# Performance work log

Measured on AMD Instinct MI355X. Metric: run time of the kernel, lower is better.

## Reference

```python
import jax, jax.numpy as jnp
import numpy as np

N_NODES = 100000
N_EDGES = 1200000
D = 64          # hidden_feat_dim == out_feat_dim
D_CELL = 16     # cell_feat_dim
HID = 256       # MLP hidden width (from MLP(..., 256, ...))
N_TGT = 50000


def setup_inputs() -> dict:
    key = jax.random.key(0)
    ks = jax.random.split(key, 13)
    inv = lambda d: 1.0 / np.sqrt(d)
    return {
        "h": jax.random.normal(ks[0], (N_NODES, D), jnp.float32),
        "cell_feat": jax.random.normal(ks[1], (N_NODES, D_CELL), jnp.float32),
        "src": jax.random.randint(ks[2], (N_EDGES,), 0, N_NODES, jnp.int32),
        "dst": jax.random.randint(ks[3], (N_EDGES,), 0, N_NODES, jnp.int32),
        "targets": jax.random.randint(ks[4], (N_TGT,), 0, N_NODES, jnp.int32),
        "Wn1": jax.random.normal(ks[5], (D, HID), jnp.float32) * inv(D),
        "bn1": jnp.zeros((HID,), jnp.float32),
        "Wn2": jax.random.normal(ks[6], (HID, D), jnp.float32) * inv(HID),
        "bn2": jnp.zeros((D,), jnp.float32),
        "Ws1": jax.random.normal(ks[7], (D_CELL, HID), jnp.float32) * inv(D_CELL),
        "bs1": jnp.zeros((HID,), jnp.float32),
        "Ws2": jax.random.normal(ks[8], (HID, D), jnp.float32) * inv(HID),
        "bs2": jnp.zeros((D,), jnp.float32),
    }


def _mlp2(x, W1, b1, W2, b2):
    # MLP(d_in, 256, d_out) with LeakyReLU(negative_slope=0) == ReLU
    return jax.nn.relu(x @ W1 + b1) @ W2 + b2


def reference(h, cell_feat, src, dst, targets,
              Wn1, bn1, Wn2, bn2, Ws1, bs1, Ws2, bs2):
    # PathConv forward, even level_id > 0, flag_attn=False:
    #   pull(copy_src('h','m'), cell_msg_reduce, apply_cell_func) on 'cell' edges
    N = h.shape[0]
    m = h[src]  # gather edge messages [E, D]
    # cell_msg_reduce: per-dst, per-channel softmax over incoming messages
    mmax = jax.ops.segment_max(m, dst, num_segments=N)          # [N, D]
    mmax = jnp.where(jnp.isfinite(mmax), mmax, 0.0)             # isolated nodes
    e = jnp.exp(m - mmax[dst])                                  # [E, D]
    den = jax.ops.segment_sum(e, dst, num_segments=N)           # [N, D]
    num = jax.ops.segment_sum(e * m, dst, num_segments=N)       # sum(msg*softmax)
    h_neigh1 = num / jnp.where(den == 0.0, 1.0, den)            # [N, D]
    # apply_cell_func: fc_cell_self(cell_feat) + fc_cell_neigh(h_neigh1)
    h_new = _mlp2(cell_feat, Ws1, bs1, Ws2, bs2) + _mlp2(h_neigh1, Wn1, bn1, Wn2, bn2)
    h_new = jax.nn.relu(h_new)  # self.activation
    return h_new[targets]
```

## Files before the change

kernel.cpp:

```cpp
#include <hip/hip_runtime.h>

#define NN 100000
#define NE 1200000
#define DD 64
#define DC 16
#define DH 256
#define NT 50000
#define MAXDEG 64

typedef __attribute__((ext_vector_type(8))) short bf16x8;
typedef __attribute__((ext_vector_type(4))) short bf16x4;
typedef __attribute__((ext_vector_type(4))) float f32x4;

__device__ __forceinline__ unsigned short f2bf(float x) {
    unsigned int u = __float_as_uint(x);
    return (unsigned short)((u + 0x7FFFu + ((u >> 16) & 1u)) >> 16);
}
__device__ __forceinline__ float bf2f(unsigned short b) {
    return __uint_as_float(((unsigned int)b) << 16);
}

__device__ __forceinline__ void split8r(const float* p, bf16x8& hi, bf16x8& lo) {
    f32x4 a = *reinterpret_cast<const f32x4*>(p);
    f32x4 b = *reinterpret_cast<const f32x4*>(p + 4);
    #pragma unroll
    for (int j = 0; j < 4; ++j) {
        unsigned short h = f2bf(a[j]);
        hi[j] = (short)h;
        lo[j] = (short)f2bf(a[j] - bf2f(h));
    }
    #pragma unroll
    for (int j = 0; j < 4; ++j) {
        unsigned short h = f2bf(b[j]);
        hi[4 + j] = (short)h;
        lo[4 + j] = (short)f2bf(b[j] - bf2f(h));
    }
}

__device__ __forceinline__ bf16x8 zero8() {
    return bf16x8{0, 0, 0, 0, 0, 0, 0, 0};
}
__device__ __forceinline__ bf16x8 pad8(bf16x4 v) {
    return bf16x8{v[0], v[1], v[2], v[3], 0, 0, 0, 0};
}

__global__ __launch_bounds__(256) void mark_wl_k(
    const int* __restrict__ tg, int* __restrict__ ifl, int* __restrict__ cnt)
{
    int i = blockIdx.x * 256 + threadIdx.x;
    int lane = threadIdx.x & 63;
    bool claim = false;
    int t = 0;
    if (i < NT) {
        t = tg[i];
        claim = (atomicCAS(&ifl[t], -1, -2) == -1);
    }
    unsigned long long mask = __ballot(claim);
    if (mask == 0ull) return;
    int nclaim = __popcll(mask);
    int leader = __ffsll((unsigned long long)mask) - 1;
    int base = 0;
    if (lane == leader) base = atomicAdd(cnt, nclaim);
    base = __shfl(base, leader);
    if (claim) {
        int rank = __popcll(mask & ((1ull << lane) - 1ull));
        ifl[t] = base + rank;
    }
}

__global__ __launch_bounds__(256) void scatter_k(
    const int* __restrict__ src, const int* __restrict__ dst,
    const int* __restrict__ ifl, int* __restrict__ deg, int* __restrict__ csr)
{
    int e = blockIdx.x * 256 + threadIdx.x;
    if (e >= NE) return;
    int d = dst[e];
    int w = ifl[d];
    if (w >= 0) {
        int slot = atomicAdd(&deg[w], 1);
        if (slot < MAXDEG) csr[w * MAXDEG + slot] = src[e];
    }
}

__global__ __launch_bounds__(256) void reduce_k(
    const float* __restrict__ h, const int* __restrict__ csr,
    const int* __restrict__ deg, const int* __restrict__ cnt,
    float* __restrict__ hn_c)
{
    int gw = (blockIdx.x * 256 + threadIdx.x) >> 6;
    int lane = threadIdx.x & 63;
    if (gw >= cnt[0]) return;
    int g = min(deg[gw], MAXDEG);
    int sid = csr[gw * MAXDEG + lane];
    if (lane >= g) sid = 0;
    const int e4 = lane >> 4, c4 = lane & 15;

    f32x4 accd = {0.f, 0.f, 0.f, 0.f}, accn = {0.f, 0.f, 0.f, 0.f};
    for (int base = 0; base < g; base += 16) {
        f32x4 m[4];
        bool  val[4];
        #pragma unroll
        for (int bb = 0; bb < 4; ++bb) {
            int idx = base + bb * 4 + e4;
            val[bb] = (idx < g);
            if (base + bb * 4 < g) {
                int s = __shfl(sid, idx);
                m[bb] = *reinterpret_cast<const f32x4*>(
                            h + (size_t)s * DD + c4 * 4);
            } else {
                m[bb] = f32x4{0.f, 0.f, 0.f, 0.f};
                val[bb] = false;
            }
        }
        #pragma unroll
        for (int bb = 0; bb < 4; ++bb) {
            #pragma unroll
            for (int r = 0; r < 4; ++r) {
                float ex = __expf(m[bb][r]);
                ex = val[bb] ? ex : 0.f;
                accd[r] += ex;
                accn[r] = fmaf(ex, m[bb][r], accn[r]);
            }
        }
    }
    #pragma unroll
    for (int r = 0; r < 4; ++r) {
        accd[r] += __shfl_xor(accd[r], 16);
        accn[r] += __shfl_xor(accn[r], 16);
        accd[r] += __shfl_xor(accd[r], 32);
        accn[r] += __shfl_xor(accn[r], 32);
    }
    if (lane < 16) {
        f32x4 o;
        #pragma unroll
        for (int r = 0; r < 4; ++r)
            o[r] = (accd[r] == 0.f) ? 0.f : accn[r] / accd[r];
        *reinterpret_cast<f32x4*>(hn_c + (size_t)gw * DD + c4 * 4) = o;
    }
}

#define N_W1NT 16384
#define N_W1ST 8192
#define N_W2N  16384
#define N_W2S  16384
#define N_PACK (N_W1NT + N_W1ST + N_W2N + N_W2S)

__global__ __launch_bounds__(256) void pack_w_k(
    const float* __restrict__ Wn1, const float* __restrict__ Ws1,
    const float* __restrict__ Wn2, const float* __restrict__ Ws2,
    unsigned short* __restrict__ W1nT_hi, unsigned short* __restrict__ W1nT_lo,
    unsigned short* __restrict__ W1sT_hi, unsigned short* __restrict__ W1sT_lo,
    unsigned short* __restrict__ W2n_hi,  unsigned short* __restrict__ W2n_lo,
    unsigned short* __restrict__ W2s_hi,  unsigned short* __restrict__ W2s_lo)
{
    int tid = blockIdx.x * 256 + threadIdx.x;
    if (tid >= N_PACK) return;
    float v; unsigned short *ph, *pl; int idx;
    if (tid < N_W1NT) {
        idx = tid;
        int j = idx & 7, l = (idx >> 3) & 63, rest = idx >> 9;
        int ks = rest & 1, c = rest >> 1;
        int feat = ks * 32 + ((l >> 4) << 3) + j, hid = (c << 4) + (l & 15);
        v = Wn1[(size_t)feat * DH + hid];
        ph = W1nT_hi; pl = W1nT_lo;
    } else if (tid < N_W1NT + N_W1ST) {
        idx = tid - N_W1NT;
        int j = idx & 7, l = (idx >> 3) & 63, c = idx >> 9;
        int k = ((l >> 4) << 3) + j, hid = (c << 4) + (l & 15);
        v = (k < DC) ? Ws1[(size_t)k * DH + hid] : 0.0f;
        ph = W1sT_hi; pl = W1sT_lo;
    } else if (tid < N_W1NT + N_W1ST + N_W2N) {
        idx = tid - N_W1NT - N_W1ST;
        int j = idx & 3, l = (idx >> 2) & 63, rest = idx >> 8;
        int u = rest & 3, c = rest >> 2;
        int row = (c << 4) + ((l >> 4) << 2) + j, col = (u << 4) + (l & 15);
        v = Wn2[(size_t)row * DD + col];
        ph = W2n_hi; pl = W2n_lo;
    } else {
        idx = tid - N_W1NT - N_W1ST - N_W2N;
        int j = idx & 3, l = (idx >> 2) & 63, rest = idx >> 8;
        int u = rest & 3, c = rest >> 2;
        int row = (c << 4) + ((l >> 4) << 2) + j, col = (u << 4) + (l & 15);
        v = Ws2[(size_t)row * DD + col];
        ph = W2s_hi; pl = W2s_lo;
    }
    unsigned short hh = f2bf(v);
    ph[idx] = hh;
    pl[idx] = f2bf(v - bf2f(hh));
}

__global__ __launch_bounds__(256, 4) void mfma_mlp_k(
    const float* __restrict__ hn_c, const int* __restrict__ ifl,
    const float* __restrict__ cellf, const int* __restrict__ tg,
    const unsigned short* __restrict__ W1nT_hi, const unsigned short* __restrict__ W1nT_lo,
    const unsigned short* __restrict__ W1sT_hi, const unsigned short* __restrict__ W1sT_lo,
    const unsigned short* __restrict__ W2n_hi,  const unsigned short* __restrict__ W2n_lo,
    const unsigned short* __restrict__ W2s_hi,  const unsigned short* __restrict__ W2s_lo,
    const float* __restrict__ bn1, const float* __restrict__ bs1,
    const float* __restrict__ bn2, const float* __restrict__ bs2,
    float* __restrict__ out)
{
    __shared__ float X[32][84];
    __shared__ float Ys[4][16][68];

    const int tid = threadIdx.x;
    const int wv = tid >> 6, ln = tid & 63;
    const int l16 = ln & 15, kb = (ln >> 4) << 3;
    const int rbase = blockIdx.x * 32;

    {
        int r = tid >> 3, seg = tid & 7;
        int row = rbase + r; if (row >= NT) row = NT - 1;
        int t = tg[row];
        int w = ifl[t];
        const float* hp = hn_c + (size_t)w * DD + seg * 8;
        *reinterpret_cast<f32x4*>(&X[r][seg * 8])     = *reinterpret_cast<const f32x4*>(hp);
        *reinterpret_cast<f32x4*>(&X[r][seg * 8 + 4]) = *reinterpret_cast<const f32x4*>(hp + 4);
        if (tid < 128) {
            int r2 = tid >> 2, q = tid & 3;
            int row2 = rbase + r2; if (row2 >= NT) row2 = NT - 1;
            int t2 = tg[row2];
            *reinterpret_cast<f32x4*>(&X[r2][64 + q * 4]) =
                *reinterpret_cast<const f32x4*>(cellf + (size_t)t2 * DC + q * 4);
        }
    }
    __syncthreads();

    f32x4 accY[2][4];
    #pragma unroll
    for (int g = 0; g < 2; ++g)
        #pragma unroll
        for (int u = 0; u < 4; ++u) accY[g][u] = f32x4{0.f, 0.f, 0.f, 0.f};

    {
        bf16x8 xh[2][2], xl[2][2];
        #pragma unroll
        for (int g = 0; g < 2; ++g)
            #pragma unroll
            for (int ks = 0; ks < 2; ++ks)
                split8r(&X[g * 16 + l16][ks * 32 + kb], xh[g][ks], xl[g][ks]);

        #pragma unroll
        for (int cc = 0; cc < 4; ++cc) {
            int cg = (wv << 2) + cc;
            f32x4 b1 = *reinterpret_cast<const f32x4*>(bn1 + cg * 16 + ((ln >> 4) << 2));
            f32x4 a1[2] = {b1, b1};
            #pragma unroll
            for (int ks = 0; ks < 2; ++ks) {
                bf16x8 wh = *reinterpret_cast<const bf16x8*>(W1nT_hi + (((cg * 2 + ks) * 64 + ln) << 3));
                bf16x8 wl = *reinterpret_cast<const bf16x8*>(W1nT_lo + (((cg * 2 + ks) * 64 + ln) << 3));
                #pragma unroll
                for (int g = 0; g < 2; ++g) {
                    a1[g] = __builtin_amdgcn_mfma_f32_16x16x32_bf16(wh, xh[g][ks], a1[g], 0, 0, 0);
                    a1[g] = __builtin_amdgcn_mfma_f32_16x16x32_bf16(wl, xh[g][ks], a1[g], 0, 0, 0);
                    a1[g] = __builtin_amdgcn_mfma_f32_16x16x32_bf16(wh, xl[g][ks], a1[g], 0, 0, 0);
                }
            }
            bf16x8 pah[2], pal[2];
            #pragma unroll
            for (int g = 0; g < 2; ++g) {
                pah[g] = zero8(); pal[g] = zero8();
                #pragma unroll
                for (int r = 0; r < 4; ++r) {
                    float d = fmaxf(a1[g][r], 0.f);
                    unsigned short hh = f2bf(d);
                    pah[g][r] = (short)hh;
                    pal[g][r] = (short)f2bf(d - bf2f(hh));
                }
            }
            #pragma unroll
            for (int u = 0; u < 4; ++u) {
                bf16x8 w2h = pad8(*reinterpret_cast<const bf16x4*>(W2n_hi + (((cg * 4 + u) * 64 + ln) << 2)));
                bf16x8 w2l = pad8(*reinterpret_cast<const bf16x4*>(W2n_lo + (((cg * 4 + u) * 64 + ln) << 2)));
                #pragma unroll
                for (int g = 0; g < 2; ++g) {
                    accY[g][u] = __builtin_amdgcn_mfma_f32_16x16x32_bf16(pah[g], w2h, accY[g][u], 0, 0, 0);
                    accY[g][u] = __builtin_amdgcn_mfma_f32_16x16x32_bf16(pal[g], w2h, accY[g][u], 0, 0, 0);
                    accY[g][u] = __builtin_amdgcn_mfma_f32_16x16x32_bf16(pah[g], w2l, accY[g][u], 0, 0, 0);
                }
            }
        }
    }

    {
        bf16x8 sxh[2], sxl[2];
        #pragma unroll
        for (int g = 0; g < 2; ++g) { sxh[g] = zero8(); sxl[g] = zero8(); }
        if (ln < 32) {
            #pragma unroll
            for (int g = 0; g < 2; ++g)
                split8r(&X[g * 16 + l16][64 + kb], sxh[g], sxl[g]);
        }
        #pragma unroll
        for (int cc = 0; cc < 4; ++cc) {
            int cg = (wv << 2) + cc;
            f32x4 b1 = *reinterpret_cast<const f32x4*>(bs1 + cg * 16 + ((ln >> 4) << 2));
            f32x4 a1[2] = {b1, b1};
            {
                bf16x8 wh = *reinterpret_cast<const bf16x8*>(W1sT_hi + ((cg * 64 + ln) << 3));
                bf16x8 wl = *reinterpret_cast<const bf16x8*>(W1sT_lo + ((cg * 64 + ln) << 3));
                #pragma unroll
                for (int g = 0; g < 2; ++g) {
                    a1[g] = __builtin_amdgcn_mfma_f32_16x16x32_bf16(wh, sxh[g], a1[g], 0, 0, 0);
                    a1[g] = __builtin_amdgcn_mfma_f32_16x16x32_bf16(wl, sxh[g], a1[g], 0, 0, 0);
                    a1[g] = __builtin_amdgcn_mfma_f32_16x16x32_bf16(wh, sxl[g], a1[g], 0, 0, 0);
                }
            }
            bf16x8 pah[2], pal[2];
            #pragma unroll
            for (int g = 0; g < 2; ++g) {
                pah[g] = zero8(); pal[g] = zero8();
                #pragma unroll
                for (int r = 0; r < 4; ++r) {
                    float d = fmaxf(a1[g][r], 0.f);
                    unsigned short hh = f2bf(d);
                    pah[g][r] = (short)hh;
                    pal[g][r] = (short)f2bf(d - bf2f(hh));
                }
            }
            #pragma unroll
            for (int u = 0; u < 4; ++u) {
                bf16x8 w2h = pad8(*reinterpret_cast<const bf16x4*>(W2s_hi + (((cg * 4 + u) * 64 + ln) << 2)));
                bf16x8 w2l = pad8(*reinterpret_cast<const bf16x4*>(W2s_lo + (((cg * 4 + u) * 64 + ln) << 2)));
                #pragma unroll
                for (int g = 0; g < 2; ++g) {
                    accY[g][u] = __builtin_amdgcn_mfma_f32_16x16x32_bf16(pah[g], w2h, accY[g][u], 0, 0, 0);
                    accY[g][u] = __builtin_amdgcn_mfma_f32_16x16x32_bf16(pal[g], w2h, accY[g][u], 0, 0, 0);
                    accY[g][u] = __builtin_amdgcn_mfma_f32_16x16x32_bf16(pah[g], w2l, accY[g][u], 0, 0, 0);
                }
            }
        }
    }

    #pragma unroll
    for (int g = 0; g < 2; ++g) {
        #pragma unroll
        for (int u = 0; u < 4; ++u)
            #pragma unroll
            for (int r = 0; r < 4; ++r)
                Ys[wv][(ln >> 4) * 4 + r][u * 16 + l16] = accY[g][u][r];
        __syncthreads();
        {
            int row = tid >> 4, cs = tid & 15;
            f32x4 s = {0.f, 0.f, 0.f, 0.f};
            #pragma unroll
            for (int wq = 0; wq < 4; ++wq)
                s += *reinterpret_cast<const f32x4*>(&Ys[wq][row][cs * 4]);
            f32x4 c0 = *reinterpret_cast<const f32x4*>(bn2 + cs * 4);
            f32x4 c1 = *reinterpret_cast<const f32x4*>(bs2 + cs * 4);
            #pragma unroll
            for (int j = 0; j < 4; ++j) s[j] = fmaxf(s[j] + c0[j] + c1[j], 0.f);
            int rowg = rbase + g * 16 + row;
            if (rowg < NT)
                *reinterpret_cast<f32x4*>(out + (size_t)rowg * DD + cs * 4) = s;
        }
        __syncthreads();
    }
}

extern "C" void kernel_launch(void* const* d_in, const int* in_sizes, int n_in,
                              void* d_out, int out_size, void* d_ws, size_t ws_size,
                              hipStream_t stream)
{
    const float* h     = (const float*)d_in[0];
    const float* cellf = (const float*)d_in[1];
    const int*   src   = (const int*)d_in[2];
    const int*   dst   = (const int*)d_in[3];
    const int*   tg    = (const int*)d_in[4];
    const float* Wn1   = (const float*)d_in[5];
    const float* bn1   = (const float*)d_in[6];
    const float* Wn2   = (const float*)d_in[7];
    const float* bn2   = (const float*)d_in[8];
    const float* Ws1   = (const float*)d_in[9];
    const float* bs1   = (const float*)d_in[10];
    const float* Ws2   = (const float*)d_in[11];
    const float* bs2   = (const float*)d_in[12];
    float* out = (float*)d_out;

    int*   ifl  = (int*)d_ws;
    int*   deg  = ifl + NN;
    int*   cnt  = deg + NT;
    int*   csr  = cnt + 16;
    float* hn_c = (float*)(csr + (size_t)NT * MAXDEG);
    size_t woff = ((size_t)((char*)(hn_c + (size_t)NT * DD) - (char*)d_ws) + 63)
                  & ~(size_t)63;
    unsigned short* W1nT_hi = (unsigned short*)((char*)d_ws + woff);
    unsigned short* W1nT_lo = W1nT_hi + N_W1NT;
    unsigned short* W1sT_hi = W1nT_lo + N_W1NT;
    unsigned short* W1sT_lo = W1sT_hi + N_W1ST;
    unsigned short* W2n_hi  = W1sT_lo + N_W1ST;
    unsigned short* W2n_lo  = W2n_hi + N_W2N;
    unsigned short* W2s_hi  = W2n_lo + N_W2N;
    unsigned short* W2s_lo  = W2s_hi + N_W2S;

    hipMemsetAsync(ifl, 0xFF, NN * sizeof(int), stream);
    hipMemsetAsync(deg, 0, (NT + 16) * sizeof(int), stream);

    pack_w_k<<<(N_PACK + 255) / 256, 256, 0, stream>>>(
        Wn1, Ws1, Wn2, Ws2, W1nT_hi, W1nT_lo, W1sT_hi, W1sT_lo,
        W2n_hi, W2n_lo, W2s_hi, W2s_lo);

    mark_wl_k<<<(NT + 255) / 256, 256, 0, stream>>>(tg, ifl, cnt);

    scatter_k<<<(NE + 255) / 256, 256, 0, stream>>>(src, dst, ifl, deg, csr);

    reduce_k<<<NT / 4, 256, 0, stream>>>(h, csr, deg, cnt, hn_c);

    mfma_mlp_k<<<(NT + 31) / 32, 256, 0, stream>>>(hn_c, ifl, cellf, tg,
        W1nT_hi, W1nT_lo, W1sT_hi, W1sT_lo, W2n_hi, W2n_lo, W2s_hi, W2s_lo,
        bn1, bs1, bn2, bs2, out);
}
```

Measured before the change: 105.3 us.

## Drop weight lo-parts, keep weights in registers, persistent double-buffered MLP

Weights are now stored as a single bf16 copy instead of hi/lo pairs, which cuts the MFMA count per product from three to two and halves the packed weight traffic. Activations are still split into hi/lo, but with truncation rather than round-to-nearest. The MLP kernel becomes persistent with a fixed grid of 512 blocks: weights are loaded into registers once per block, and the gathered input rows for the next tile are prefetched while the current tile computes. The cost is lower accuracy from bf16-only weights and higher register pressure, with the occupancy bound lowered to 2.

New measurement: 124.1 us. 1.18x slower.

```diff
diff --git a/kernel.cpp b/kernel.cpp
--- a/kernel.cpp
+++ b/kernel.cpp
@@ -7,6 +7,8 @@
 #define DH 256
 #define NT 50000
 #define MAXDEG 64
+#define GRID_MLP 512
+#define NTILES ((NT + 31) / 32)
 
 typedef __attribute__((ext_vector_type(8))) short bf16x8;
 typedef __attribute__((ext_vector_type(4))) short bf16x4;
@@ -20,20 +22,20 @@
     return __uint_as_float(((unsigned int)b) << 16);
 }
 
-__device__ __forceinline__ void split8r(const float* p, bf16x8& hi, bf16x8& lo) {
+__device__ __forceinline__ void split8t(const float* p, bf16x8& hi, bf16x8& lo) {
     f32x4 a = *reinterpret_cast<const f32x4*>(p);
     f32x4 b = *reinterpret_cast<const f32x4*>(p + 4);
     #pragma unroll
     for (int j = 0; j < 4; ++j) {
-        unsigned short h = f2bf(a[j]);
+        unsigned short h = (unsigned short)(__float_as_uint(a[j]) >> 16);
         hi[j] = (short)h;
-        lo[j] = (short)f2bf(a[j] - bf2f(h));
+        lo[j] = (short)(__float_as_uint(a[j] - bf2f(h)) >> 16);
     }
     #pragma unroll
     for (int j = 0; j < 4; ++j) {
-        unsigned short h = f2bf(b[j]);
+        unsigned short h = (unsigned short)(__float_as_uint(b[j]) >> 16);
         hi[4 + j] = (short)h;
-        lo[4 + j] = (short)f2bf(b[j] - bf2f(h));
+        lo[4 + j] = (short)(__float_as_uint(b[j] - bf2f(h)) >> 16);
     }
 }
 
@@ -148,97 +150,138 @@
 __global__ __launch_bounds__(256) void pack_w_k(
     const float* __restrict__ Wn1, const float* __restrict__ Ws1,
     const float* __restrict__ Wn2, const float* __restrict__ Ws2,
-    unsigned short* __restrict__ W1nT_hi, unsigned short* __restrict__ W1nT_lo,
-    unsigned short* __restrict__ W1sT_hi, unsigned short* __restrict__ W1sT_lo,
-    unsigned short* __restrict__ W2n_hi,  unsigned short* __restrict__ W2n_lo,
-    unsigned short* __restrict__ W2s_hi,  unsigned short* __restrict__ W2s_lo)
+    unsigned short* __restrict__ W1nT, unsigned short* __restrict__ W1sT,
+    unsigned short* __restrict__ W2n,  unsigned short* __restrict__ W2s)
 {
     int tid = blockIdx.x * 256 + threadIdx.x;
     if (tid >= N_PACK) return;
-    float v; unsigned short *ph, *pl; int idx;
+    float v; unsigned short* ph; int idx;
     if (tid < N_W1NT) {
         idx = tid;
         int j = idx & 7, l = (idx >> 3) & 63, rest = idx >> 9;
         int ks = rest & 1, c = rest >> 1;
         int feat = ks * 32 + ((l >> 4) << 3) + j, hid = (c << 4) + (l & 15);
         v = Wn1[(size_t)feat * DH + hid];
-        ph = W1nT_hi; pl = W1nT_lo;
+        ph = W1nT;
     } else if (tid < N_W1NT + N_W1ST) {
         idx = tid - N_W1NT;
         int j = idx & 7, l = (idx >> 3) & 63, c = idx >> 9;
         int k = ((l >> 4) << 3) + j, hid = (c << 4) + (l & 15);
         v = (k < DC) ? Ws1[(size_t)k * DH + hid] : 0.0f;
-        ph = W1sT_hi; pl = W1sT_lo;
+        ph = W1sT;
     } else if (tid < N_W1NT + N_W1ST + N_W2N) {
         idx = tid - N_W1NT - N_W1ST;
         int j = idx & 3, l = (idx >> 2) & 63, rest = idx >> 8;
         int u = rest & 3, c = rest >> 2;
         int row = (c << 4) + ((l >> 4) << 2) + j, col = (u << 4) + (l & 15);
         v = Wn2[(size_t)row * DD + col];
-        ph = W2n_hi; pl = W2n_lo;
+        ph = W2n;
     } else {
         idx = tid - N_W1NT - N_W1ST - N_W2N;
         int j = idx & 3, l = (idx >> 2) & 63, rest = idx >> 8;
         int u = rest & 3, c = rest >> 2;
         int row = (c << 4) + ((l >> 4) << 2) + j, col = (u << 4) + (l & 15);
         v = Ws2[(size_t)row * DD + col];
-        ph = W2s_hi; pl = W2s_lo;
-    }
-    unsigned short hh = f2bf(v);
-    ph[idx] = hh;
-    pl[idx] = f2bf(v - bf2f(hh));
-}
-
-__global__ __launch_bounds__(256, 4) void mfma_mlp_k(
+        ph = W2s;
+    }
+    ph[idx] = f2bf(v);
+}
+
+__global__ __launch_bounds__(256, 2) void mfma_mlp_k(
     const float* __restrict__ hn_c, const int* __restrict__ ifl,
     const float* __restrict__ cellf, const int* __restrict__ tg,
-    const unsigned short* __restrict__ W1nT_hi, const unsigned short* __restrict__ W1nT_lo,
-    const unsigned short* __restrict__ W1sT_hi, const unsigned short* __restrict__ W1sT_lo,
-    const unsigned short* __restrict__ W2n_hi,  const unsigned short* __restrict__ W2n_lo,
-    const unsigned short* __restrict__ W2s_hi,  const unsigned short* __restrict__ W2s_lo,
+    const unsigned short* __restrict__ W1nT, const unsigned short* __restrict__ W1sT,
+    const unsigned short* __restrict__ W2n,  const unsigned short* __restrict__ W2s,
     const float* __restrict__ bn1, const float* __restrict__ bs1,
     const float* __restrict__ bn2, const float* __restrict__ bs2,
     float* __restrict__ out)
 {
-    __shared__ float X[32][84];
+    __shared__ float X[2][32][84];
     __shared__ float Ys[4][16][68];
 
     const int tid = threadIdx.x;
     const int wv = tid >> 6, ln = tid & 63;
     const int l16 = ln & 15, kb = (ln >> 4) << 3;
-    const int rbase = blockIdx.x * 32;
-
+
+    bf16x8 wn1[4][2]; bf16x8 ws1v[4]; bf16x4 w2nv[4][4], w2sv[4][4];
+    #pragma unroll
+    for (int cc = 0; cc < 4; ++cc) {
+        int cg = (wv << 2) + cc;
+        #pragma unroll
+        for (int ks = 0; ks < 2; ++ks)
+            wn1[cc][ks] = *reinterpret_cast<const bf16x8*>(
+                W1nT + (((cg * 2 + ks) * 64 + ln) << 3));
+        ws1v[cc] = *reinterpret_cast<const bf16x8*>(W1sT + ((cg * 64 + ln) << 3));
+        #pragma unroll
+        for (int u = 0; u < 4; ++u) {
+            w2nv[cc][u] = *reinterpret_cast<const bf16x4*>(
+                W2n + (((cg * 4 + u) * 64 + ln) << 2));
+            w2sv[cc][u] = *reinterpret_cast<const bf16x4*>(
+                W2s + (((cg * 4 + u) * 64 + ln) << 2));
+        }
+    }
+    f32x4 b2p;
     {
+        int cs = tid & 15;
+        f32x4 c0 = *reinterpret_cast<const f32x4*>(bn2 + cs * 4);
+        f32x4 c1 = *reinterpret_cast<const f32x4*>(bs2 + cs * 4);
+        #pragma unroll
+        for (int j = 0; j < 4; ++j) b2p[j] = c0[j] + c1[j];
+    }
+
+    {
+        int tile = blockIdx.x;
         int r = tid >> 3, seg = tid & 7;
-        int row = rbase + r; if (row >= NT) row = NT - 1;
-        int t = tg[row];
-        int w = ifl[t];
+        int row = tile * 32 + r; if (row >= NT) row = NT - 1;
+        int t = tg[row]; int w = ifl[t];
         const float* hp = hn_c + (size_t)w * DD + seg * 8;
-        *reinterpret_cast<f32x4*>(&X[r][seg * 8])     = *reinterpret_cast<const f32x4*>(hp);
-        *reinterpret_cast<f32x4*>(&X[r][seg * 8 + 4]) = *reinterpret_cast<const f32x4*>(hp + 4);
+        *reinterpret_cast<f32x4*>(&X[0][r][seg * 8])     = *reinterpret_cast<const f32x4*>(hp);
+        *reinterpret_cast<f32x4*>(&X[0][r][seg * 8 + 4]) = *reinterpret_cast<const f32x4*>(hp + 4);
         if (tid < 128) {
             int r2 = tid >> 2, q = tid & 3;
-            int row2 = rbase + r2; if (row2 >= NT) row2 = NT - 1;
+            int row2 = tile * 32 + r2; if (row2 >= NT) row2 = NT - 1;
             int t2 = tg[row2];
-            *reinterpret_cast<f32x4*>(&X[r2][64 + q * 4]) =
+            *reinterpret_cast<f32x4*>(&X[0][r2][64 + q * 4]) =
                 *reinterpret_cast<const f32x4*>(cellf + (size_t)t2 * DC + q * 4);
         }
     }
     __syncthreads();
 
-    f32x4 accY[2][4];
-    #pragma unroll
-    for (int g = 0; g < 2; ++g)
-        #pragma unroll
-        for (int u = 0; u < 4; ++u) accY[g][u] = f32x4{0.f, 0.f, 0.f, 0.f};
-
-    {
-        bf16x8 xh[2][2], xl[2][2];
+    int cur = 0;
+    for (int tile = blockIdx.x; tile < NTILES; tile += GRID_MLP) {
+        bf16x8 xh[2][2], xl[2][2], sxh[2], sxl[2];
+        #pragma unroll
+        for (int g = 0; g < 2; ++g) {
+            #pragma unroll
+            for (int ks = 0; ks < 2; ++ks)
+                split8t(&X[cur][g * 16 + l16][ks * 32 + kb], xh[g][ks], xl[g][ks]);
+            sxh[g] = zero8(); sxl[g] = zero8();
+            if (ln < 32)
+                split8t(&X[cur][g * 16 + l16][64 + kb], sxh[g], sxl[g]);
+        }
+
+        const bool have_next = (tile + GRID_MLP < NTILES);
+        f32x4 sv0, sv1, sc;
+        if (have_next) {
+            int r = tid >> 3, seg = tid & 7;
+            int row = (tile + GRID_MLP) * 32 + r; if (row >= NT) row = NT - 1;
+            int t = tg[row]; int w = ifl[t];
+            const float* hp = hn_c + (size_t)w * DD + seg * 8;
+            sv0 = *reinterpret_cast<const f32x4*>(hp);
+            sv1 = *reinterpret_cast<const f32x4*>(hp + 4);
+            if (tid < 128) {
+                int r2 = tid >> 2, q = tid & 3;
+                int row2 = (tile + GRID_MLP) * 32 + r2; if (row2 >= NT) row2 = NT - 1;
+                int t2 = tg[row2];
+                sc = *reinterpret_cast<const f32x4*>(cellf + (size_t)t2 * DC + q * 4);
+            }
+        }
+
+        f32x4 accY[2][4];
         #pragma unroll
         for (int g = 0; g < 2; ++g)
             #pragma unroll
-            for (int ks = 0; ks < 2; ++ks)
-                split8r(&X[g * 16 + l16][ks * 32 + kb], xh[g][ks], xl[g][ks]);
+            for (int u = 0; u < 4; ++u) accY[g][u] = f32x4{0.f, 0.f, 0.f, 0.f};
 
         #pragma unroll
         for (int cc = 0; cc < 4; ++cc) {
@@ -246,16 +289,12 @@
             f32x4 b1 = *reinterpret_cast<const f32x4*>(bn1 + cg * 16 + ((ln >> 4) << 2));
             f32x4 a1[2] = {b1, b1};
             #pragma unroll
-            for (int ks = 0; ks < 2; ++ks) {
-                bf16x8 wh = *reinterpret_cast<const bf16x8*>(W1nT_hi + (((cg * 2 + ks) * 64 + ln) << 3));
-                bf16x8 wl = *reinterpret_cast<const bf16x8*>(W1nT_lo + (((cg * 2 + ks) * 64 + ln) << 3));
+            for (int ks = 0; ks < 2; ++ks)
                 #pragma unroll
                 for (int g = 0; g < 2; ++g) {
-                    a1[g] = __builtin_amdgcn_mfma_f32_16x16x32_bf16(wh, xh[g][ks], a1[g], 0, 0, 0);
-                    a1[g] = __builtin_amdgcn_mfma_f32_16x16x32_bf16(wl, xh[g][ks], a1[g], 0, 0, 0);
-                    a1[g] = __builtin_amdgcn_mfma_f32_16x16x32_bf16(wh, xl[g][ks], a1[g], 0, 0, 0);
+                    a1[g] = __builtin_amdgcn_mfma_f32_16x16x32_bf16(wn1[cc][ks], xh[g][ks], a1[g], 0, 0, 0);
+                    a1[g] = __builtin_amdgcn_mfma_f32_16x16x32_bf16(wn1[cc][ks], xl[g][ks], a1[g], 0, 0, 0);
                 }
-            }
             bf16x8 pah[2], pal[2];
             #pragma unroll
             for (int g = 0; g < 2; ++g) {
@@ -263,48 +302,31 @@
                 #pragma unroll
                 for (int r = 0; r < 4; ++r) {
                     float d = fmaxf(a1[g][r], 0.f);
-                    unsigned short hh = f2bf(d);
+                    unsigned short hh = (unsigned short)(__float_as_uint(d) >> 16);
                     pah[g][r] = (short)hh;
-                    pal[g][r] = (short)f2bf(d - bf2f(hh));
+                    pal[g][r] = (short)(__float_as_uint(d - bf2f(hh)) >> 16);
                 }
             }
             #pragma unroll
             for (int u = 0; u < 4; ++u) {
-                bf16x8 w2h = pad8(*reinterpret_cast<const bf16x4*>(W2n_hi + (((cg * 4 + u) * 64 + ln) << 2)));
-                bf16x8 w2l = pad8(*reinterpret_cast<const bf16x4*>(W2n_lo + (((cg * 4 + u) * 64 + ln) << 2)));
+                bf16x8 wp = pad8(w2nv[cc][u]);
                 #pragma unroll
                 for (int g = 0; g < 2; ++g) {
-                    accY[g][u] = __builtin_amdgcn_mfma_f32_16x16x32_bf16(pah[g], w2h, accY[g][u], 0, 0, 0);
-                    accY[g][u] = __builtin_amdgcn_mfma_f32_16x16x32_bf16(pal[g], w2h, accY[g][u], 0, 0, 0);
-                    accY[g][u] = __builtin_amdgcn_mfma_f32_16x16x32_bf16(pah[g], w2l, accY[g][u], 0, 0, 0);
+                    accY[g][u] = __builtin_amdgcn_mfma_f32_16x16x32_bf16(pah[g], wp, accY[g][u], 0, 0, 0);
+                    accY[g][u] = __builtin_amdgcn_mfma_f32_16x16x32_bf16(pal[g], wp, accY[g][u], 0, 0, 0);
                 }
             }
         }
-    }
-
-    {
-        bf16x8 sxh[2], sxl[2];
-        #pragma unroll
-        for (int g = 0; g < 2; ++g) { sxh[g] = zero8(); sxl[g] = zero8(); }
-        if (ln < 32) {
-            #pragma unroll
-            for (int g = 0; g < 2; ++g)
-                split8r(&X[g * 16 + l16][64 + kb], sxh[g], sxl[g]);
-        }
+
         #pragma unroll
         for (int cc = 0; cc < 4; ++cc) {
             int cg = (wv << 2) + cc;
             f32x4 b1 = *reinterpret_cast<const f32x4*>(bs1 + cg * 16 + ((ln >> 4) << 2));
             f32x4 a1[2] = {b1, b1};
-            {
-                bf16x8 wh = *reinterpret_cast<const bf16x8*>(W1sT_hi + ((cg * 64 + ln) << 3));
-                bf16x8 wl = *reinterpret_cast<const bf16x8*>(W1sT_lo + ((cg * 64 + ln) << 3));
-                #pragma unroll
-                for (int g = 0; g < 2; ++g) {
-                    a1[g] = __builtin_amdgcn_mfma_f32_16x16x32_bf16(wh, sxh[g], a1[g], 0, 0, 0);
-                    a1[g] = __builtin_amdgcn_mfma_f32_16x16x32_bf16(wl, sxh[g], a1[g], 0, 0, 0);
-                    a1[g] = __builtin_amdgcn_mfma_f32_16x16x32_bf16(wh, sxl[g], a1[g], 0, 0, 0);
-                }
+            #pragma unroll
+            for (int g = 0; g < 2; ++g) {
+                a1[g] = __builtin_amdgcn_mfma_f32_16x16x32_bf16(ws1v[cc], sxh[g], a1[g], 0, 0, 0);
+                a1[g] = __builtin_amdgcn_mfma_f32_16x16x32_bf16(ws1v[cc], sxl[g], a1[g], 0, 0, 0);
             }
             bf16x8 pah[2], pal[2];
             #pragma unroll
@@ -313,48 +335,56 @@
                 #pragma unroll
                 for (int r = 0; r < 4; ++r) {
                     float d = fmaxf(a1[g][r], 0.f);
-                    unsigned short hh = f2bf(d);
+                    unsigned short hh = (unsigned short)(__float_as_uint(d) >> 16);
                     pah[g][r] = (short)hh;
-                    pal[g][r] = (short)f2bf(d - bf2f(hh));
+                    pal[g][r] = (short)(__float_as_uint(d - bf2f(hh)) >> 16);
                 }
             }
             #pragma unroll
             for (int u = 0; u < 4; ++u) {
-                bf16x8 w2h = pad8(*reinterpret_cast<const bf16x4*>(W2s_hi + (((cg * 4 + u) * 64 + ln) << 2)));
-                bf16x8 w2l = pad8(*reinterpret_cast<const bf16x4*>(W2s_lo + (((cg * 4 + u) * 64 + ln) << 2)));
+                bf16x8 wp = pad8(w2sv[cc][u]);
                 #pragma unroll
                 for (int g = 0; g < 2; ++g) {
-                    accY[g][u] = __builtin_amdgcn_mfma_f32_16x16x32_bf16(pah[g], w2h, accY[g][u], 0, 0, 0);
-                    accY[g][u] = __builtin_amdgcn_mfma_f32_16x16x32_bf16(pal[g], w2h, accY[g][u], 0, 0, 0);
-                    accY[g][u] = __builtin_amdgcn_mfma_f32_16x16x32_bf16(pah[g], w2l, accY[g][u], 0, 0, 0);
+                    accY[g][u] = __builtin_amdgcn_mfma_f32_16x16x32_bf16(pah[g], wp, accY[g][u], 0, 0, 0);
+                    accY[g][u] = __builtin_amdgcn_mfma_f32_16x16x32_bf16(pal[g], wp, accY[g][u], 0, 0, 0);
                 }
             }
         }
-    }
-
-    #pragma unroll
-    for (int g = 0; g < 2; ++g) {
-        #pragma unroll
-        for (int u = 0; u < 4; ++u)
-            #pragma unroll
-            for (int r = 0; r < 4; ++r)
-                Ys[wv][(ln >> 4) * 4 + r][u * 16 + l16] = accY[g][u][r];
-        __syncthreads();
-        {
-            int row = tid >> 4, cs = tid & 15;
-            f32x4 s = {0.f, 0.f, 0.f, 0.f};
-            #pragma unroll
-            for (int wq = 0; wq < 4; ++wq)
-                s += *reinterpret_cast<const f32x4*>(&Ys[wq][row][cs * 4]);
-            f32x4 c0 = *reinterpret_cast<const f32x4*>(bn2 + cs * 4);
-            f32x4 c1 = *reinterpret_cast<const f32x4*>(bs2 + cs * 4);
-            #pragma unroll
-            for (int j = 0; j < 4; ++j) s[j] = fmaxf(s[j] + c0[j] + c1[j], 0.f);
-            int rowg = rbase + g * 16 + row;
-            if (rowg < NT)
-                *reinterpret_cast<f32x4*>(out + (size_t)rowg * DD + cs * 4) = s;
-        }
-        __syncthreads();
+
+        #pragma unroll
+        for (int g = 0; g < 2; ++g) {
+            #pragma unroll
+            for (int u = 0; u < 4; ++u)
+                #pragma unroll
+                for (int r = 0; r < 4; ++r)
+                    Ys[wv][(ln >> 4) * 4 + r][u * 16 + l16] = accY[g][u][r];
+            __syncthreads();
+            {
+                int row = tid >> 4, cs = tid & 15;
+                f32x4 s = {0.f, 0.f, 0.f, 0.f};
+                #pragma unroll
+                for (int wq = 0; wq < 4; ++wq)
+                    s += *reinterpret_cast<const f32x4*>(&Ys[wq][row][cs * 4]);
+                #pragma unroll
+                for (int j = 0; j < 4; ++j) s[j] = fmaxf(s[j] + b2p[j], 0.f);
+                int rowg = tile * 32 + g * 16 + row;
+                if (rowg < NT)
+                    *reinterpret_cast<f32x4*>(out + (size_t)rowg * DD + cs * 4) = s;
+            }
+            __syncthreads();
+        }
+
+        if (have_next) {
+            int r = tid >> 3, seg = tid & 7;
+            *reinterpret_cast<f32x4*>(&X[cur ^ 1][r][seg * 8])     = sv0;
+            *reinterpret_cast<f32x4*>(&X[cur ^ 1][r][seg * 8 + 4]) = sv1;
+            if (tid < 128) {
+                int r2 = tid >> 2, q = tid & 3;
+                *reinterpret_cast<f32x4*>(&X[cur ^ 1][r2][64 + q * 4]) = sc;
+            }
+            __syncthreads();
+        }
+        cur ^= 1;
     }
 }
 
@@ -384,21 +414,16 @@
     float* hn_c = (float*)(csr + (size_t)NT * MAXDEG);
     size_t woff = ((size_t)((char*)(hn_c + (size_t)NT * DD) - (char*)d_ws) + 63)
                   & ~(size_t)63;
-    unsigned short* W1nT_hi = (unsigned short*)((char*)d_ws + woff);
-    unsigned short* W1nT_lo = W1nT_hi + N_W1NT;
-    unsigned short* W1sT_hi = W1nT_lo + N_W1NT;
-    unsigned short* W1sT_lo = W1sT_hi + N_W1ST;
-    unsigned short* W2n_hi  = W1sT_lo + N_W1ST;
-    unsigned short* W2n_lo  = W2n_hi + N_W2N;
-    unsigned short* W2s_hi  = W2n_lo + N_W2N;
-    unsigned short* W2s_lo  = W2s_hi + N_W2S;
+    unsigned short* W1nT = (unsigned short*)((char*)d_ws + woff);
+    unsigned short* W1sT = W1nT + N_W1NT;
+    unsigned short* W2n  = W1sT + N_W1ST;
+    unsigned short* W2s  = W2n + N_W2N;
 
     hipMemsetAsync(ifl, 0xFF, NN * sizeof(int), stream);
     hipMemsetAsync(deg, 0, (NT + 16) * sizeof(int), stream);
 
     pack_w_k<<<(N_PACK + 255) / 256, 256, 0, stream>>>(
-        Wn1, Ws1, Wn2, Ws2, W1nT_hi, W1nT_lo, W1sT_hi, W1sT_lo,
-        W2n_hi, W2n_lo, W2s_hi, W2s_lo);
+        Wn1, Ws1, Wn2, Ws2, W1nT, W1sT, W2n, W2s);
 
     mark_wl_k<<<(NT + 255) / 256, 256, 0, stream>>>(tg, ifl, cnt);
 
@@ -406,7 +431,6 @@
 
     reduce_k<<<NT / 4, 256, 0, stream>>>(h, csr, deg, cnt, hn_c);
 
-    mfma_mlp_k<<<(NT + 31) / 32, 256, 0, stream>>>(hn_c, ifl, cellf, tg,
-        W1nT_hi, W1nT_lo, W1sT_hi, W1sT_lo, W2n_hi, W2n_lo, W2s_hi, W2s_lo,
-        bn1, bs1, bn2, bs2, out);
-}
+    mfma_mlp_k<<<GRID_MLP, 256, 0, stream>>>(hn_c, ifl, cellf, tg,
+        W1nT, W1sT, W2n, W2s, bn1, bs1, bn2, bs2, out);
+}
```
